# Optimization experiments

Measured on AMD Instinct MI355X. Metric: run time of the kernel, lower is better.

## Reference

```python
import jax, jax.numpy as jnp
import numpy as np

D = 2048
B = 4
L = 2048  # new tokens
S = 2048  # cached tokens


def setup_inputs() -> dict:
    key = jax.random.key(0)
    ks = jax.random.split(key, 6)
    scale = 1.0 / np.sqrt(D)
    return {
        "x": jax.random.normal(ks[0], (B, L, D), dtype=jnp.float32),
        "cache_k": jax.random.normal(ks[1], (B, S, D), dtype=jnp.float32),
        "cache_v": jax.random.normal(ks[2], (B, S, D), dtype=jnp.float32),
        "Wq": jax.random.normal(ks[3], (D, D), dtype=jnp.float32) * scale,
        "Wk": jax.random.normal(ks[4], (D, D), dtype=jnp.float32) * scale,
        "Wv": jax.random.normal(ks[5], (D, D), dtype=jnp.float32) * scale,
    }


def reference(x, cache_k, cache_v, Wq, Wk, Wv):
    # nn.Linear(D, D, bias=False): y = x @ W.T
    Q = jnp.einsum("bld,ed->ble", x, Wq)
    K = jnp.einsum("bld,ed->ble", x, Wk)
    V = jnp.einsum("bld,ed->ble", x, Wv)
    # Faithful to source: new K/V are PREPENDED to the existing cache
    K_cal = jnp.concatenate([K, cache_k], axis=1)  # [B, L+S, D]
    V_cal = jnp.concatenate([V, cache_v], axis=1)
    inv_scale = 1.0 / jnp.sqrt(jnp.float32(D))
    scores = jnp.einsum("bld,bsd->bls", Q, K_cal) * inv_scale  # [B, L, L+S]
    attn = jax.nn.softmax(scores, axis=-1)
    out = jnp.einsum("bls,bsd->bld", attn, V_cal)  # [B, L, D]
    return out
```

## Files before the change

### kernel.cpp

```cpp
#include <hip/hip_runtime.h>
#include <hip/hip_bf16.h>
#include <cstdint>
#include <cstddef>

typedef __bf16 bf16_t;
typedef __bf16 bf16x4 __attribute__((ext_vector_type(4)));
typedef __bf16 bf16x8 __attribute__((ext_vector_type(8)));
typedef float f32x4 __attribute__((ext_vector_type(4)));

#define DEV __device__ __forceinline__

DEV void async16(const void* g, void* l) {
  __builtin_amdgcn_global_load_lds(
      (const __attribute__((address_space(1))) void*)g,
      (__attribute__((address_space(3))) void*)l, 16, 0, 0);
}

DEV void store_out(float* p, float v) { *p = v; }
DEV void store_out(bf16_t* p, float v) { *p = (bf16_t)v; }

template <typename OutT>
__global__ __launch_bounds__(256) void gemm_bt(
    const bf16_t* __restrict__ A, int lda,
    const bf16_t* __restrict__ B, int ldb,
    OutT* __restrict__ C, int ldc,
    int K, float scale) {
  __shared__ bf16_t As[128 * 64];
  __shared__ bf16_t Bs[128 * 64];

  const int tid = threadIdx.x;
  const int m0 = blockIdx.y * 128;
  const int n0 = blockIdx.x * 128;
  const int w = tid >> 6, lane = tid & 63;
  const int wr = w >> 1, wc = w & 1;
  const int lr = lane & 15;
  const int lk8 = (lane >> 4) * 8;

  const bf16_t* ga[4];
  const bf16_t* gb[4];
#pragma unroll
  for (int i = 0; i < 4; ++i) {
    int c = i * 256 + tid;
    int r = c >> 3, col = (c & 7) * 8;
    ga[i] = A + (size_t)(m0 + r) * lda + col;
    gb[i] = B + (size_t)(n0 + r) * ldb + col;
  }

  f32x4 acc[4][4] = {};

  for (int k0 = 0; k0 < K; k0 += 64) {
    __syncthreads();
#pragma unroll
    for (int i = 0; i < 4; ++i) {
      int c = i * 256 + tid;
      async16(ga[i], &As[c * 8]);
      async16(gb[i], &Bs[c * 8]);
      ga[i] += 64;
      gb[i] += 64;
    }
    __syncthreads();
#pragma unroll
    for (int kk = 0; kk < 2; ++kk) {
      bf16x8 af[4], bfr[4];
#pragma unroll
      for (int m = 0; m < 4; ++m)
        af[m] = *(const bf16x8*)&As[(wr * 64 + m * 16 + lr) * 64 + kk * 32 + lk8];
#pragma unroll
      for (int n = 0; n < 4; ++n)
        bfr[n] = *(const bf16x8*)&Bs[(wc * 64 + n * 16 + lr) * 64 + kk * 32 + lk8];
#pragma unroll
      for (int m = 0; m < 4; ++m)
#pragma unroll
        for (int n = 0; n < 4; ++n)
          acc[m][n] = __builtin_amdgcn_mfma_f32_16x16x32_bf16(af[m], bfr[n],
                                                              acc[m][n], 0, 0, 0);
    }
  }

  const int row0 = m0 + wr * 64 + (lane >> 4) * 4;
  const int col0 = n0 + wc * 64 + lr;
#pragma unroll
  for (int m = 0; m < 4; ++m)
#pragma unroll
    for (int n = 0; n < 4; ++n)
#pragma unroll
      for (int j = 0; j < 4; ++j) {
        float v = acc[m][n][j] * scale;
        store_out(&C[(size_t)(row0 + m * 16 + j) * ldc + (col0 + n * 16)], v);
      }
}

__global__ __launch_bounds__(256) void gemm_qkv(
    const bf16_t* __restrict__ A,
    const bf16_t* W0, const bf16_t* W1, const bf16_t* W2,
    bf16_t* C0, bf16_t* C1, bf16_t* C2) {
  __shared__ bf16_t As[128 * 64];
  __shared__ bf16_t Bs[128 * 64];

  const int z = blockIdx.z;
  const bf16_t* B = (z == 0) ? W0 : (z == 1) ? W1 : W2;
  bf16_t* C = (z == 0) ? C0 : (z == 1) ? C1 : C2;

  const int tid = threadIdx.x;
  const int m0 = blockIdx.y * 128;
  const int n0 = blockIdx.x * 128;
  const int w = tid >> 6, lane = tid & 63;
  const int wr = w >> 1, wc = w & 1;
  const int lr = lane & 15;
  const int lk8 = (lane >> 4) * 8;

  const bf16_t* ga[4];
  const bf16_t* gb[4];
#pragma unroll
  for (int i = 0; i < 4; ++i) {
    int c = i * 256 + tid;
    int r = c >> 3, col = (c & 7) * 8;
    ga[i] = A + (size_t)(m0 + r) * 2048 + col;
    gb[i] = B + (size_t)(n0 + r) * 2048 + col;
  }

  f32x4 acc[4][4] = {};

  for (int k0 = 0; k0 < 2048; k0 += 64) {
    __syncthreads();
#pragma unroll
    for (int i = 0; i < 4; ++i) {
      int c = i * 256 + tid;
      async16(ga[i], &As[c * 8]);
      async16(gb[i], &Bs[c * 8]);
      ga[i] += 64;
      gb[i] += 64;
    }
    __syncthreads();
#pragma unroll
    for (int kk = 0; kk < 2; ++kk) {
      bf16x8 af[4], bfr[4];
#pragma unroll
      for (int m = 0; m < 4; ++m)
        af[m] = *(const bf16x8*)&As[(wr * 64 + m * 16 + lr) * 64 + kk * 32 + lk8];
#pragma unroll
      for (int n = 0; n < 4; ++n)
        bfr[n] = *(const bf16x8*)&Bs[(wc * 64 + n * 16 + lr) * 64 + kk * 32 + lk8];
#pragma unroll
      for (int m = 0; m < 4; ++m)
#pragma unroll
        for (int n = 0; n < 4; ++n)
          acc[m][n] = __builtin_amdgcn_mfma_f32_16x16x32_bf16(af[m], bfr[n],
                                                              acc[m][n], 0, 0, 0);
    }
  }

  const int row0 = m0 + wr * 64 + (lane >> 4) * 4;
  const int col0 = n0 + wc * 64 + lr;
#pragma unroll
  for (int m = 0; m < 4; ++m)
#pragma unroll
    for (int n = 0; n < 4; ++n)
#pragma unroll
      for (int j = 0; j < 4; ++j)
        C[(size_t)(row0 + m * 16 + j) * 2048 + (col0 + n * 16)] =
            (bf16_t)acc[m][n][j];
}

__global__ __launch_bounds__(256) void cast_f32_bf16(
    const float* __restrict__ src, bf16_t* __restrict__ dst, int n4) {
  int i = blockIdx.x * 256 + threadIdx.x;
  if (i >= n4) return;
  float4 v = ((const float4*)src)[i];
  bf16x4 o = {(bf16_t)v.x, (bf16_t)v.y, (bf16_t)v.z, (bf16_t)v.w};
  ((bf16x4*)dst)[i] = o;
}

template <typename SrcT>
__global__ __launch_bounds__(256) void transpose_to_vt(
    const SrcT* __restrict__ src, int sLd,
    bf16_t* __restrict__ dst, int dLd, int dColOff) {
  __shared__ bf16_t tile[32][33];
  const int c0 = blockIdx.x * 32;
  const int r0 = blockIdx.y * 32;
  const int tx = threadIdx.x, ty = threadIdx.y;
#pragma unroll
  for (int j = 0; j < 4; ++j) {
    int r = r0 + ty + j * 8;
    tile[ty + j * 8][tx] = (bf16_t)(float)src[(size_t)r * sLd + c0 + tx];
  }
  __syncthreads();
#pragma unroll
  for (int j = 0; j < 4; ++j) {
    int d = c0 + ty + j * 8;
    dst[(size_t)d * dLd + dColOff + r0 + tx] = tile[tx][ty + j * 8];
  }
}

__global__ __launch_bounds__(256) void softmax_inplace(float* __restrict__ scores) {
  float* row = scores + (size_t)blockIdx.x * 4096;
  const int t = threadIdx.x;
  const int w = t >> 6, lane = t & 63;
  float4 v[4];
  float mx = -3.0e38f;
#pragma unroll
  for (int i = 0; i < 4; ++i) {
    v[i] = *(const float4*)(row + (size_t)(i * 256 + t) * 4);
    mx = fmaxf(mx, fmaxf(fmaxf(v[i].x, v[i].y), fmaxf(v[i].z, v[i].w)));
  }
#pragma unroll
  for (int o = 32; o > 0; o >>= 1) mx = fmaxf(mx, __shfl_xor(mx, o, 64));
  __shared__ float redm[4], reds[4];
  if (lane == 0) redm[w] = mx;
  __syncthreads();
  mx = fmaxf(fmaxf(redm[0], redm[1]), fmaxf(redm[2], redm[3]));
  const float LOG2E = 1.4426950408889634f;
  float e[16];
  float sum = 0.f;
#pragma unroll
  for (int i = 0; i < 4; ++i) {
    e[i * 4 + 0] = exp2f((v[i].x - mx) * LOG2E);
    e[i * 4 + 1] = exp2f((v[i].y - mx) * LOG2E);
    e[i * 4 + 2] = exp2f((v[i].z - mx) * LOG2E);
    e[i * 4 + 3] = exp2f((v[i].w - mx) * LOG2E);
    sum += e[i * 4] + e[i * 4 + 1] + e[i * 4 + 2] + e[i * 4 + 3];
  }
#pragma unroll
  for (int o = 32; o > 0; o >>= 1) sum += __shfl_xor(sum, o, 64);
  if (lane == 0) reds[w] = sum;
  __syncthreads();
  sum = reds[0] + reds[1] + reds[2] + reds[3];
  float inv = 1.0f / sum;
  bf16_t* orow = (bf16_t*)row;
#pragma unroll
  for (int i = 0; i < 4; ++i) {
    bf16x4 o4 = {(bf16_t)(e[i * 4 + 0] * inv), (bf16_t)(e[i * 4 + 1] * inv),
                 (bf16_t)(e[i * 4 + 2] * inv), (bf16_t)(e[i * 4 + 3] * inv)};
    *(bf16x4*)(orow + (size_t)(i * 256 + t) * 4) = o4;
  }
}

extern "C" void kernel_launch(void* const* d_in, const int* in_sizes, int n_in,
                              void* d_out, int out_size, void* d_ws, size_t ws_size,
                              hipStream_t stream) {
  const float* x = (const float*)d_in[0];
  const float* cK = (const float*)d_in[1];
  const float* cV = (const float*)d_in[2];
  const float* Wq = (const float*)d_in[3];
  const float* Wk = (const float*)d_in[4];
  const float* Wv = (const float*)d_in[5];
  float* out = (float*)d_out;

  char* ws = (char*)d_ws;
  bf16_t* wqb  = (bf16_t*)(ws + 0);
  bf16_t* wkb  = (bf16_t*)(ws + 8388608);
  bf16_t* wvb  = (bf16_t*)(ws + 16777216);
  bf16_t* xb   = (bf16_t*)(ws + 25165824);
  bf16_t* Qb   = (bf16_t*)(ws + 33554432);
  bf16_t* Kcal = (bf16_t*)(ws + 41943040);
  bf16_t* Vt   = (bf16_t*)(ws + 58720256);
  float*  Sc   = (float*)(ws + 75497472);
  bf16_t* Vtmp = (bf16_t*)(ws + 75497472);

  const float inv_scale = 0.022097086912079608f;
  const size_t MB4 = 4194304;

  cast_f32_bf16<<<4096, 256, 0, stream>>>(Wq, wqb, 1048576);
  cast_f32_bf16<<<4096, 256, 0, stream>>>(Wk, wkb, 1048576);
  cast_f32_bf16<<<4096, 256, 0, stream>>>(Wv, wvb, 1048576);

  for (int b = 0; b < 4; ++b) {
    const float* x_b  = x  + (size_t)b * MB4;
    const float* cK_b = cK + (size_t)b * MB4;
    const float* cV_b = cV + (size_t)b * MB4;
    float* out_b = out + (size_t)b * MB4;

    cast_f32_bf16<<<4096, 256, 0, stream>>>(x_b, xb, 1048576);
    cast_f32_bf16<<<4096, 256, 0, stream>>>(cK_b, Kcal + MB4, 1048576);
    transpose_to_vt<float><<<dim3(64, 64, 1), dim3(32, 8), 0, stream>>>(
        cV_b, 2048, Vt, 4096, 2048);

    gemm_qkv<<<dim3(16, 16, 3), 256, 0, stream>>>(xb, wqb, wkb, wvb,
                                                  Qb, Kcal, Vtmp);
    transpose_to_vt<bf16_t><<<dim3(64, 64, 1), dim3(32, 8), 0, stream>>>(
        Vtmp, 2048, Vt, 4096, 0);

    gemm_bt<float><<<dim3(32, 16, 1), 256, 0, stream>>>(
        Qb, 2048, Kcal, 2048, Sc, 4096, 2048, inv_scale);

    softmax_inplace<<<2048, 256, 0, stream>>>(Sc);

    gemm_bt<float><<<dim3(16, 16, 1), 256, 0, stream>>>(
        (const bf16_t*)Sc, 8192, Vt, 4096, out_b, 2048, 4096, 1.0f);
  }
}
```

Measured before the change: 1.233 ms.

## Batch QKV and attention GEMMs across batches and use 8-wave GEMM blocks

Switches the GEMM kernels to 512-thread blocks (8 waves, each computing a 32x64 slice) and adds batched-z variants. When the workspace is large enough, the inputs for all four batches are cast and transposed in single launches, QKV is projected in one grid covering all batches, and the score/softmax/PV stages run over batch pairs. The goal is fewer launches, larger grids for better CU occupancy, and more waves per CU to hide latency. The cost is a larger workspace, and it falls back to the per-batch loop when the workspace is too small.

```diff
diff --git a/kernel.cpp b/kernel.cpp
--- a/kernel.cpp
+++ b/kernel.cpp
@@ -16,43 +16,40 @@
       (__attribute__((address_space(3))) void*)l, 16, 0, 0);
 }
 
-DEV void store_out(float* p, float v) { *p = v; }
-DEV void store_out(bf16_t* p, float v) { *p = (bf16_t)v; }
-
-template <typename OutT>
-__global__ __launch_bounds__(256) void gemm_bt(
-    const bf16_t* __restrict__ A, int lda,
-    const bf16_t* __restrict__ B, int ldb,
-    OutT* __restrict__ C, int ldc,
+__global__ __launch_bounds__(512) void gemm_bt8(
+    const bf16_t* __restrict__ A, size_t sA, int lda,
+    const bf16_t* __restrict__ B, size_t sB, int ldb,
+    float* __restrict__ C, size_t sC, int ldc,
     int K, float scale) {
   __shared__ bf16_t As[128 * 64];
   __shared__ bf16_t Bs[128 * 64];
 
   const int tid = threadIdx.x;
-  const int m0 = blockIdx.y * 128;
-  const int n0 = blockIdx.x * 128;
+  A += (size_t)blockIdx.z * sA;
+  B += (size_t)blockIdx.z * sB;
+  C += (size_t)blockIdx.z * sC;
+  const int m0 = blockIdx.y * 128, n0 = blockIdx.x * 128;
   const int w = tid >> 6, lane = tid & 63;
   const int wr = w >> 1, wc = w & 1;
-  const int lr = lane & 15;
-  const int lk8 = (lane >> 4) * 8;
-
-  const bf16_t* ga[4];
-  const bf16_t* gb[4];
-#pragma unroll
-  for (int i = 0; i < 4; ++i) {
-    int c = i * 256 + tid;
+  const int lr = lane & 15, lk8 = (lane >> 4) * 8;
+
+  const bf16_t* ga[2];
+  const bf16_t* gb[2];
+#pragma unroll
+  for (int i = 0; i < 2; ++i) {
+    int c = i * 512 + tid;
     int r = c >> 3, col = (c & 7) * 8;
     ga[i] = A + (size_t)(m0 + r) * lda + col;
     gb[i] = B + (size_t)(n0 + r) * ldb + col;
   }
 
-  f32x4 acc[4][4] = {};
+  f32x4 acc[2][4] = {};
 
   for (int k0 = 0; k0 < K; k0 += 64) {
     __syncthreads();
 #pragma unroll
-    for (int i = 0; i < 4; ++i) {
-      int c = i * 256 + tid;
+    for (int i = 0; i < 2; ++i) {
+      int c = i * 512 + tid;
       async16(ga[i], &As[c * 8]);
       async16(gb[i], &Bs[c * 8]);
       ga[i] += 64;
@@ -61,15 +58,15 @@
     __syncthreads();
 #pragma unroll
     for (int kk = 0; kk < 2; ++kk) {
-      bf16x8 af[4], bfr[4];
-#pragma unroll
-      for (int m = 0; m < 4; ++m)
-        af[m] = *(const bf16x8*)&As[(wr * 64 + m * 16 + lr) * 64 + kk * 32 + lk8];
+      bf16x8 af[2], bfr[4];
+#pragma unroll
+      for (int m = 0; m < 2; ++m)
+        af[m] = *(const bf16x8*)&As[(wr * 32 + m * 16 + lr) * 64 + kk * 32 + lk8];
 #pragma unroll
       for (int n = 0; n < 4; ++n)
         bfr[n] = *(const bf16x8*)&Bs[(wc * 64 + n * 16 + lr) * 64 + kk * 32 + lk8];
 #pragma unroll
-      for (int m = 0; m < 4; ++m)
+      for (int m = 0; m < 2; ++m)
 #pragma unroll
         for (int n = 0; n < 4; ++n)
           acc[m][n] = __builtin_amdgcn_mfma_f32_16x16x32_bf16(af[m], bfr[n],
@@ -77,20 +74,19 @@
     }
   }
 
-  const int row0 = m0 + wr * 64 + (lane >> 4) * 4;
+  const int row0 = m0 + wr * 32 + (lane >> 4) * 4;
   const int col0 = n0 + wc * 64 + lr;
 #pragma unroll
-  for (int m = 0; m < 4; ++m)
+  for (int m = 0; m < 2; ++m)
 #pragma unroll
     for (int n = 0; n < 4; ++n)
 #pragma unroll
-      for (int j = 0; j < 4; ++j) {
-        float v = acc[m][n][j] * scale;
-        store_out(&C[(size_t)(row0 + m * 16 + j) * ldc + (col0 + n * 16)], v);
-      }
-}
-
-__global__ __launch_bounds__(256) void gemm_qkv(
+      for (int j = 0; j < 4; ++j)
+        C[(size_t)(row0 + m * 16 + j) * ldc + (col0 + n * 16)] =
+            acc[m][n][j] * scale;
+}
+
+__global__ __launch_bounds__(512) void gemm_qkv8(
     const bf16_t* __restrict__ A,
     const bf16_t* W0, const bf16_t* W1, const bf16_t* W2,
     bf16_t* C0, bf16_t* C1, bf16_t* C2) {
@@ -102,30 +98,29 @@
   bf16_t* C = (z == 0) ? C0 : (z == 1) ? C1 : C2;
 
   const int tid = threadIdx.x;
-  const int m0 = blockIdx.y * 128;
-  const int n0 = blockIdx.x * 128;
+  const int m0 = blockIdx.y * 128, n0 = blockIdx.x * 128;
+  const size_t cextra = (z == 1) ? (size_t)(m0 >> 11) * 4194304 : 0;
   const int w = tid >> 6, lane = tid & 63;
   const int wr = w >> 1, wc = w & 1;
-  const int lr = lane & 15;
-  const int lk8 = (lane >> 4) * 8;
-
-  const bf16_t* ga[4];
-  const bf16_t* gb[4];
-#pragma unroll
-  for (int i = 0; i < 4; ++i) {
-    int c = i * 256 + tid;
+  const int lr = lane & 15, lk8 = (lane >> 4) * 8;
+
+  const bf16_t* ga[2];
+  const bf16_t* gb[2];
+#pragma unroll
+  for (int i = 0; i < 2; ++i) {
+    int c = i * 512 + tid;
     int r = c >> 3, col = (c & 7) * 8;
     ga[i] = A + (size_t)(m0 + r) * 2048 + col;
     gb[i] = B + (size_t)(n0 + r) * 2048 + col;
   }
 
-  f32x4 acc[4][4] = {};
+  f32x4 acc[2][4] = {};
 
   for (int k0 = 0; k0 < 2048; k0 += 64) {
     __syncthreads();
 #pragma unroll
-    for (int i = 0; i < 4; ++i) {
-      int c = i * 256 + tid;
+    for (int i = 0; i < 2; ++i) {
+      int c = i * 512 + tid;
       async16(ga[i], &As[c * 8]);
       async16(gb[i], &Bs[c * 8]);
       ga[i] += 64;
@@ -134,15 +129,15 @@
     __syncthreads();
 #pragma unroll
     for (int kk = 0; kk < 2; ++kk) {
-      bf16x8 af[4], bfr[4];
-#pragma unroll
-      for (int m = 0; m < 4; ++m)
-        af[m] = *(const bf16x8*)&As[(wr * 64 + m * 16 + lr) * 64 + kk * 32 + lk8];
+      bf16x8 af[2], bfr[4];
+#pragma unroll
+      for (int m = 0; m < 2; ++m)
+        af[m] = *(const bf16x8*)&As[(wr * 32 + m * 16 + lr) * 64 + kk * 32 + lk8];
 #pragma unroll
       for (int n = 0; n < 4; ++n)
         bfr[n] = *(const bf16x8*)&Bs[(wc * 64 + n * 16 + lr) * 64 + kk * 32 + lk8];
 #pragma unroll
-      for (int m = 0; m < 4; ++m)
+      for (int m = 0; m < 2; ++m)
 #pragma unroll
         for (int n = 0; n < 4; ++n)
           acc[m][n] = __builtin_amdgcn_mfma_f32_16x16x32_bf16(af[m], bfr[n],
@@ -150,15 +145,15 @@
     }
   }
 
-  const int row0 = m0 + wr * 64 + (lane >> 4) * 4;
+  const int row0 = m0 + wr * 32 + (lane >> 4) * 4;
   const int col0 = n0 + wc * 64 + lr;
 #pragma unroll
-  for (int m = 0; m < 4; ++m)
+  for (int m = 0; m < 2; ++m)
 #pragma unroll
     for (int n = 0; n < 4; ++n)
 #pragma unroll
       for (int j = 0; j < 4; ++j)
-        C[(size_t)(row0 + m * 16 + j) * 2048 + (col0 + n * 16)] =
+        C[cextra + (size_t)(row0 + m * 16 + j) * 2048 + (col0 + n * 16)] =
             (bf16_t)acc[m][n][j];
 }
 
@@ -171,11 +166,24 @@
   ((bf16x4*)dst)[i] = o;
 }
 
+__global__ __launch_bounds__(256) void cast_prepend_all(
+    const float* __restrict__ src, bf16_t* __restrict__ dst) {
+  size_t i = (size_t)blockIdx.x * 256 + threadIdx.x;
+  size_t e = i * 4;
+  size_t b = e >> 22;
+  size_t within = e & ((size_t(1) << 22) - 1);
+  float4 v = *(const float4*)(src + e);
+  bf16x4 o = {(bf16_t)v.x, (bf16_t)v.y, (bf16_t)v.z, (bf16_t)v.w};
+  *(bf16x4*)(dst + (b << 23) + (size_t(1) << 22) + within) = o;
+}
+
 template <typename SrcT>
 __global__ __launch_bounds__(256) void transpose_to_vt(
-    const SrcT* __restrict__ src, int sLd,
-    bf16_t* __restrict__ dst, int dLd, int dColOff) {
+    const SrcT* __restrict__ src, size_t sB, int sLd,
+    bf16_t* __restrict__ dst, size_t dB, int dLd, int dColOff) {
   __shared__ bf16_t tile[32][33];
+  src += (size_t)blockIdx.z * sB;
+  dst += (size_t)blockIdx.z * dB;
   const int c0 = blockIdx.x * 32;
   const int r0 = blockIdx.y * 32;
   const int tx = threadIdx.x, ty = threadIdx.y;
@@ -246,46 +254,80 @@
   const float* Wv = (const float*)d_in[5];
   float* out = (float*)d_out;
 
-  char* ws = (char*)d_ws;
-  bf16_t* wqb  = (bf16_t*)(ws + 0);
-  bf16_t* wkb  = (bf16_t*)(ws + 8388608);
-  bf16_t* wvb  = (bf16_t*)(ws + 16777216);
-  bf16_t* xb   = (bf16_t*)(ws + 25165824);
-  bf16_t* Qb   = (bf16_t*)(ws + 33554432);
-  bf16_t* Kcal = (bf16_t*)(ws + 41943040);
-  bf16_t* Vt   = (bf16_t*)(ws + 58720256);
-  float*  Sc   = (float*)(ws + 75497472);
-  bf16_t* Vtmp = (bf16_t*)(ws + 75497472);
-
   const float inv_scale = 0.022097086912079608f;
   const size_t MB4 = 4194304;
-
+  char* ws = (char*)d_ws;
+
+  const int tier = (ws_size >= 293601280ULL) ? 2
+                 : (ws_size >= 260046848ULL) ? 1 : 0;
+
+  bf16_t* wqb = (bf16_t*)(ws + 0);
+  bf16_t* wkb = (bf16_t*)(ws + 8388608);
+  bf16_t* wvb = (bf16_t*)(ws + 16777216);
   cast_f32_bf16<<<4096, 256, 0, stream>>>(Wq, wqb, 1048576);
   cast_f32_bf16<<<4096, 256, 0, stream>>>(Wk, wkb, 1048576);
   cast_f32_bf16<<<4096, 256, 0, stream>>>(Wv, wvb, 1048576);
 
-  for (int b = 0; b < 4; ++b) {
-    const float* x_b  = x  + (size_t)b * MB4;
-    const float* cK_b = cK + (size_t)b * MB4;
-    const float* cV_b = cV + (size_t)b * MB4;
-    float* out_b = out + (size_t)b * MB4;
-
-    cast_f32_bf16<<<4096, 256, 0, stream>>>(x_b, xb, 1048576);
-    cast_f32_bf16<<<4096, 256, 0, stream>>>(cK_b, Kcal + MB4, 1048576);
-    transpose_to_vt<float><<<dim3(64, 64, 1), dim3(32, 8), 0, stream>>>(
-        cV_b, 2048, Vt, 4096, 2048);
-
-    gemm_qkv<<<dim3(16, 16, 3), 256, 0, stream>>>(xb, wqb, wkb, wvb,
-                                                  Qb, Kcal, Vtmp);
-    transpose_to_vt<bf16_t><<<dim3(64, 64, 1), dim3(32, 8), 0, stream>>>(
-        Vtmp, 2048, Vt, 4096, 0);
-
-    gemm_bt<float><<<dim3(32, 16, 1), 256, 0, stream>>>(
-        Qb, 2048, Kcal, 2048, Sc, 4096, 2048, inv_scale);
-
-    softmax_inplace<<<2048, 256, 0, stream>>>(Sc);
-
-    gemm_bt<float><<<dim3(16, 16, 1), 256, 0, stream>>>(
-        (const bf16_t*)Sc, 8192, Vt, 4096, out_b, 2048, 4096, 1.0f);
-  }
-}
+  if (tier > 0) {
+    bf16_t* xb   = (bf16_t*)(ws + 25165824);
+    bf16_t* Qb   = (bf16_t*)(ws + 58720256);
+    bf16_t* Kcal = (bf16_t*)(ws + 92274688);
+    bf16_t* Vt   = (bf16_t*)(ws + 159383552);
+    float*  Sc   = (float*)(ws + 226492416);
+    bf16_t* Vtmp = (tier == 2) ? (bf16_t*)(ws + 260046848)
+                               : (bf16_t*)(ws + 226492416);
+    const int PAIR = (tier == 2) ? 2 : 1;
+
+    cast_f32_bf16<<<16384, 256, 0, stream>>>(x, xb, 4194304);
+    cast_prepend_all<<<16384, 256, 0, stream>>>(cK, Kcal);
+    transpose_to_vt<float><<<dim3(64, 64, 4), dim3(32, 8), 0, stream>>>(
+        cV, MB4, 2048, Vt, 8388608ULL, 4096, 2048);
+
+    gemm_qkv8<<<dim3(16, 64, 3), 512, 0, stream>>>(xb, wqb, wkb, wvb,
+                                                   Qb, Kcal, Vtmp);
+    transpose_to_vt<bf16_t><<<dim3(64, 64, 4), dim3(32, 8), 0, stream>>>(
+        Vtmp, MB4, 2048, Vt, 8388608ULL, 4096, 0);
+
+    for (int bp = 0; bp < 4; bp += PAIR) {
+      gemm_bt8<<<dim3(32, 16, PAIR), 512, 0, stream>>>(
+          Qb + (size_t)bp * MB4, MB4, 2048,
+          Kcal + (size_t)bp * 8388608, 8388608ULL, 2048,
+          Sc, 8388608ULL, 4096, 2048, inv_scale);
+      softmax_inplace<<<2048 * PAIR, 256, 0, stream>>>(Sc);
+      gemm_bt8<<<dim3(16, 16, PAIR), 512, 0, stream>>>(
+          (const bf16_t*)Sc, 16777216ULL, 8192,
+          Vt + (size_t)bp * 8388608, 8388608ULL, 4096,
+          out + (size_t)bp * MB4, MB4, 2048, 4096, 1.0f);
+    }
+  } else {
+    bf16_t* xb   = (bf16_t*)(ws + 25165824);
+    bf16_t* Qb   = (bf16_t*)(ws + 33554432);
+    bf16_t* Kcal = (bf16_t*)(ws + 41943040);
+    bf16_t* Vt   = (bf16_t*)(ws + 58720256);
+    float*  Sc   = (float*)(ws + 75497472);
+    bf16_t* Vtmp = (bf16_t*)(ws + 75497472);
+
+    for (int b = 0; b < 4; ++b) {
+      const float* x_b  = x  + (size_t)b * MB4;
+      const float* cK_b = cK + (size_t)b * MB4;
+      const float* cV_b = cV + (size_t)b * MB4;
+      float* out_b = out + (size_t)b * MB4;
+
+      cast_f32_bf16<<<4096, 256, 0, stream>>>(x_b, xb, 1048576);
+      cast_f32_bf16<<<4096, 256, 0, stream>>>(cK_b, Kcal + MB4, 1048576);
+      transpose_to_vt<float><<<dim3(64, 64, 1), dim3(32, 8), 0, stream>>>(
+          cV_b, 0, 2048, Vt, 0, 4096, 2048);
+
+      gemm_qkv8<<<dim3(16, 16, 3), 512, 0, stream>>>(xb, wqb, wkb, wvb,
+                                                     Qb, Kcal, Vtmp);
+      transpose_to_vt<bf16_t><<<dim3(64, 64, 1), dim3(32, 8), 0, stream>>>(
+          Vtmp, 0, 2048, Vt, 0, 4096, 0);
+
+      gemm_bt8<<<dim3(32, 16, 1), 512, 0, stream>>>(
+          Qb, 0, 2048, Kcal, 0, 2048, Sc, 0, 4096, 2048, inv_scale);
+      softmax_inplace<<<2048, 256, 0, stream>>>(Sc);
+      gemm_bt8<<<dim3(16, 16, 1), 512, 0, stream>>>(
+          (const bf16_t*)Sc, 0, 8192, Vt, 0, 4096, out_b, 0, 2048, 4096, 1.0f);
+    }
+  }
+}
```

Result: slower. 1.279 ms (+3.7%).

## Batch all four sequences into single launches and fuse V transpose into QKV GEMM

Applied to the files above, without the earlier changes.

Replaces the per-batch loop of small launches with batched kernels. Casts x and cache_k for all batches at once, and transposes cache_v for all batches at once. The QKV projection now runs as one grid over all 8192 rows and writes K directly into the concatenated cache and V directly in transposed layout, which removes the separate Vtmp transpose pass. The score GEMM runs in pairs of batches when the workspace is large enough, softmax writes to a separate bf16 buffer, and the PV GEMM is one batched launch. The goal is fewer launches and fuller GPU occupancy, at the cost of a much larger workspace and strided transposed stores in the QKV epilogue.

```diff
diff --git a/kernel.cpp b/kernel.cpp
--- a/kernel.cpp
+++ b/kernel.cpp
@@ -16,25 +16,22 @@
       (__attribute__((address_space(3))) void*)l, 16, 0, 0);
 }
 
-DEV void store_out(float* p, float v) { *p = v; }
-DEV void store_out(bf16_t* p, float v) { *p = (bf16_t)v; }
-
-template <typename OutT>
-__global__ __launch_bounds__(256) void gemm_bt(
-    const bf16_t* __restrict__ A, int lda,
-    const bf16_t* __restrict__ B, int ldb,
-    OutT* __restrict__ C, int ldc,
+__global__ __launch_bounds__(256) void gemm_bt4(
+    const bf16_t* __restrict__ A, size_t sA, int lda,
+    const bf16_t* __restrict__ B, size_t sB, int ldb,
+    float* __restrict__ C, size_t sC, int ldc,
     int K, float scale) {
   __shared__ bf16_t As[128 * 64];
   __shared__ bf16_t Bs[128 * 64];
 
   const int tid = threadIdx.x;
-  const int m0 = blockIdx.y * 128;
-  const int n0 = blockIdx.x * 128;
+  A += (size_t)blockIdx.z * sA;
+  B += (size_t)blockIdx.z * sB;
+  C += (size_t)blockIdx.z * sC;
+  const int m0 = blockIdx.y * 128, n0 = blockIdx.x * 128;
   const int w = tid >> 6, lane = tid & 63;
   const int wr = w >> 1, wc = w & 1;
-  const int lr = lane & 15;
-  const int lk8 = (lane >> 4) * 8;
+  const int lr = lane & 15, lk8 = (lane >> 4) * 8;
 
   const bf16_t* ga[4];
   const bf16_t* gb[4];
@@ -84,13 +81,12 @@
 #pragma unroll
     for (int n = 0; n < 4; ++n)
 #pragma unroll
-      for (int j = 0; j < 4; ++j) {
-        float v = acc[m][n][j] * scale;
-        store_out(&C[(size_t)(row0 + m * 16 + j) * ldc + (col0 + n * 16)], v);
-      }
-}
-
-__global__ __launch_bounds__(256) void gemm_qkv(
+      for (int j = 0; j < 4; ++j)
+        C[(size_t)(row0 + m * 16 + j) * ldc + (col0 + n * 16)] =
+            acc[m][n][j] * scale;
+}
+
+__global__ __launch_bounds__(256) void gemm_qkv4(
     const bf16_t* __restrict__ A,
     const bf16_t* W0, const bf16_t* W1, const bf16_t* W2,
     bf16_t* C0, bf16_t* C1, bf16_t* C2) {
@@ -99,15 +95,12 @@
 
   const int z = blockIdx.z;
   const bf16_t* B = (z == 0) ? W0 : (z == 1) ? W1 : W2;
-  bf16_t* C = (z == 0) ? C0 : (z == 1) ? C1 : C2;
 
   const int tid = threadIdx.x;
-  const int m0 = blockIdx.y * 128;
-  const int n0 = blockIdx.x * 128;
+  const int m0 = blockIdx.y * 128, n0 = blockIdx.x * 128;
   const int w = tid >> 6, lane = tid & 63;
   const int wr = w >> 1, wc = w & 1;
-  const int lr = lane & 15;
-  const int lk8 = (lane >> 4) * 8;
+  const int lr = lane & 15, lk8 = (lane >> 4) * 8;
 
   const bf16_t* ga[4];
   const bf16_t* gb[4];
@@ -152,14 +145,31 @@
 
   const int row0 = m0 + wr * 64 + (lane >> 4) * 4;
   const int col0 = n0 + wc * 64 + lr;
-#pragma unroll
-  for (int m = 0; m < 4; ++m)
-#pragma unroll
-    for (int n = 0; n < 4; ++n)
-#pragma unroll
-      for (int j = 0; j < 4; ++j)
-        C[(size_t)(row0 + m * 16 + j) * 2048 + (col0 + n * 16)] =
-            (bf16_t)acc[m][n][j];
+
+  if (z == 2) {
+    const size_t bb = (size_t)(m0 >> 11) * 8388608;
+    const int l0 = (row0 & 2047);
+#pragma unroll
+    for (int m = 0; m < 4; ++m)
+#pragma unroll
+      for (int n = 0; n < 4; ++n) {
+        int d = col0 + n * 16;
+        bf16x4 o4 = {(bf16_t)acc[m][n][0], (bf16_t)acc[m][n][1],
+                     (bf16_t)acc[m][n][2], (bf16_t)acc[m][n][3]};
+        *(bf16x4*)&C2[bb + (size_t)d * 4096 + l0 + m * 16] = o4;
+      }
+  } else {
+    bf16_t* C = (z == 0) ? C0 : C1;
+    const size_t cextra = (z == 1) ? (size_t)(m0 >> 11) * 4194304 : 0;
+#pragma unroll
+    for (int m = 0; m < 4; ++m)
+#pragma unroll
+      for (int n = 0; n < 4; ++n)
+#pragma unroll
+        for (int j = 0; j < 4; ++j)
+          C[cextra + (size_t)(row0 + m * 16 + j) * 2048 + (col0 + n * 16)] =
+              (bf16_t)acc[m][n][j];
+  }
 }
 
 __global__ __launch_bounds__(256) void cast_f32_bf16(
@@ -171,29 +181,43 @@
   ((bf16x4*)dst)[i] = o;
 }
 
-template <typename SrcT>
-__global__ __launch_bounds__(256) void transpose_to_vt(
-    const SrcT* __restrict__ src, int sLd,
-    bf16_t* __restrict__ dst, int dLd, int dColOff) {
+__global__ __launch_bounds__(256) void cast_prepend_all(
+    const float* __restrict__ src, bf16_t* __restrict__ dst) {
+  size_t i = (size_t)blockIdx.x * 256 + threadIdx.x;
+  size_t e = i * 4;
+  size_t b = e >> 22;
+  size_t within = e & ((size_t(1) << 22) - 1);
+  float4 v = *(const float4*)(src + e);
+  bf16x4 o = {(bf16_t)v.x, (bf16_t)v.y, (bf16_t)v.z, (bf16_t)v.w};
+  *(bf16x4*)(dst + (b << 23) + (size_t(1) << 22) + within) = o;
+}
+
+__global__ __launch_bounds__(256) void transpose_f32_to_vt(
+    const float* __restrict__ src, size_t sB, bf16_t* __restrict__ dst,
+    size_t dB, int dColOff) {
   __shared__ bf16_t tile[32][33];
+  src += (size_t)blockIdx.z * sB;
+  dst += (size_t)blockIdx.z * dB;
   const int c0 = blockIdx.x * 32;
   const int r0 = blockIdx.y * 32;
   const int tx = threadIdx.x, ty = threadIdx.y;
 #pragma unroll
   for (int j = 0; j < 4; ++j) {
     int r = r0 + ty + j * 8;
-    tile[ty + j * 8][tx] = (bf16_t)(float)src[(size_t)r * sLd + c0 + tx];
+    tile[ty + j * 8][tx] = (bf16_t)src[(size_t)r * 2048 + c0 + tx];
   }
   __syncthreads();
 #pragma unroll
   for (int j = 0; j < 4; ++j) {
     int d = c0 + ty + j * 8;
-    dst[(size_t)d * dLd + dColOff + r0 + tx] = tile[tx][ty + j * 8];
-  }
-}
-
-__global__ __launch_bounds__(256) void softmax_inplace(float* __restrict__ scores) {
-  float* row = scores + (size_t)blockIdx.x * 4096;
+    dst[(size_t)d * 4096 + dColOff + r0 + tx] = tile[tx][ty + j * 8];
+  }
+}
+
+__global__ __launch_bounds__(256) void softmax_out(
+    const float* __restrict__ src, bf16_t* __restrict__ dst) {
+  const float* row = src + (size_t)blockIdx.x * 4096;
+  bf16_t* orow = dst + (size_t)blockIdx.x * 4096;
   const int t = threadIdx.x;
   const int w = t >> 6, lane = t & 63;
   float4 v[4];
@@ -226,7 +250,6 @@
   __syncthreads();
   sum = reds[0] + reds[1] + reds[2] + reds[3];
   float inv = 1.0f / sum;
-  bf16_t* orow = (bf16_t*)row;
 #pragma unroll
   for (int i = 0; i < 4; ++i) {
     bf16x4 o4 = {(bf16_t)(e[i * 4 + 0] * inv), (bf16_t)(e[i * 4 + 1] * inv),
@@ -246,46 +269,43 @@
   const float* Wv = (const float*)d_in[5];
   float* out = (float*)d_out;
 
+  const float inv_scale = 0.022097086912079608f;
+  const size_t MB4 = 4194304;
   char* ws = (char*)d_ws;
+
   bf16_t* wqb  = (bf16_t*)(ws + 0);
   bf16_t* wkb  = (bf16_t*)(ws + 8388608);
   bf16_t* wvb  = (bf16_t*)(ws + 16777216);
   bf16_t* xb   = (bf16_t*)(ws + 25165824);
-  bf16_t* Qb   = (bf16_t*)(ws + 33554432);
-  bf16_t* Kcal = (bf16_t*)(ws + 41943040);
-  bf16_t* Vt   = (bf16_t*)(ws + 58720256);
-  float*  Sc   = (float*)(ws + 75497472);
-  bf16_t* Vtmp = (bf16_t*)(ws + 75497472);
-
-  const float inv_scale = 0.022097086912079608f;
-  const size_t MB4 = 4194304;
+  bf16_t* Qb   = (bf16_t*)(ws + 58720256);
+  bf16_t* Kcal = (bf16_t*)(ws + 92274688);
+  bf16_t* Vt   = (bf16_t*)(ws + 159383552);
+  float*  Sc   = (float*)(ws + 226492416);
+  bf16_t* Pb   = (bf16_t*)(ws + 25165824);
+  const int PAIR = (ws_size >= 293601280ULL) ? 2 : 1;
 
   cast_f32_bf16<<<4096, 256, 0, stream>>>(Wq, wqb, 1048576);
   cast_f32_bf16<<<4096, 256, 0, stream>>>(Wk, wkb, 1048576);
   cast_f32_bf16<<<4096, 256, 0, stream>>>(Wv, wvb, 1048576);
-
-  for (int b = 0; b < 4; ++b) {
-    const float* x_b  = x  + (size_t)b * MB4;
-    const float* cK_b = cK + (size_t)b * MB4;
-    const float* cV_b = cV + (size_t)b * MB4;
-    float* out_b = out + (size_t)b * MB4;
-
-    cast_f32_bf16<<<4096, 256, 0, stream>>>(x_b, xb, 1048576);
-    cast_f32_bf16<<<4096, 256, 0, stream>>>(cK_b, Kcal + MB4, 1048576);
-    transpose_to_vt<float><<<dim3(64, 64, 1), dim3(32, 8), 0, stream>>>(
-        cV_b, 2048, Vt, 4096, 2048);
-
-    gemm_qkv<<<dim3(16, 16, 3), 256, 0, stream>>>(xb, wqb, wkb, wvb,
-                                                  Qb, Kcal, Vtmp);
-    transpose_to_vt<bf16_t><<<dim3(64, 64, 1), dim3(32, 8), 0, stream>>>(
-        Vtmp, 2048, Vt, 4096, 0);
-
-    gemm_bt<float><<<dim3(32, 16, 1), 256, 0, stream>>>(
-        Qb, 2048, Kcal, 2048, Sc, 4096, 2048, inv_scale);
-
-    softmax_inplace<<<2048, 256, 0, stream>>>(Sc);
-
-    gemm_bt<float><<<dim3(16, 16, 1), 256, 0, stream>>>(
-        (const bf16_t*)Sc, 8192, Vt, 4096, out_b, 2048, 4096, 1.0f);
-  }
-}
+  cast_f32_bf16<<<16384, 256, 0, stream>>>(x, xb, 4194304);
+  cast_prepend_all<<<16384, 256, 0, stream>>>(cK, Kcal);
+  transpose_f32_to_vt<<<dim3(64, 64, 4), dim3(32, 8), 0, stream>>>(
+      cV, MB4, Vt, 8388608ULL, 2048);
+
+  gemm_qkv4<<<dim3(16, 64, 3), 256, 0, stream>>>(xb, wqb, wkb, wvb,
+                                                 Qb, Kcal, Vt);
+
+  for (int bp = 0; bp < 4; bp += PAIR) {
+    gemm_bt4<<<dim3(32, 16, PAIR), 256, 0, stream>>>(
+        Qb + (size_t)bp * MB4, MB4, 2048,
+        Kcal + (size_t)bp * 8388608, 8388608ULL, 2048,
+        Sc, 8388608ULL, 4096, 2048, inv_scale);
+    for (int q = 0; q < PAIR; ++q)
+      softmax_out<<<2048, 256, 0, stream>>>(
+          Sc + (size_t)q * 8388608, Pb + (size_t)(bp + q) * 8388608);
+  }
+
+  gemm_bt4<<<dim3(16, 16, 4), 256, 0, stream>>>(
+      Pb, 8388608ULL, 4096, Vt, 8388608ULL, 4096,
+      out, MB4, 2048, 4096, 1.0f);
+}
```

Result: faster. 1.062 ms (-13.8%).
